# Kernel tuning notes

Hardware: AMD Instinct MI355X
Metric: run time of the kernel (lower is better)

Reference implementation:

```python
import jax, jax.numpy as jnp
import numpy as np


def _normalize_xyz_with_pc(pc, xyz):
    # Center by point-cloud centroid, scale by max radius of centered cloud.
    center = pc.mean(axis=1, keepdims=True)                      # [B,1,3]
    pc_c = pc - center
    scale = jnp.sqrt((pc_c ** 2).sum(-1)).max(axis=1)            # [B]
    scale = jnp.maximum(scale, 1e-6)[:, None, None]              # [B,1,1]
    return (xyz - center) / scale


def _nn_gather(seed_n, pts_n, feat):
    # seed_n [B,M,3], pts_n [B,K,3], feat [B,C,K] -> [B,C,M]
    d2 = ((seed_n ** 2).sum(-1)[:, :, None]
          + (pts_n ** 2).sum(-1)[:, None, :]
          - 2.0 * jnp.einsum('bmd,bkd->bmk', seed_n, pts_n))     # [B,M,K]
    idx = jnp.argmin(d2, axis=-1)                                # [B,M]
    return jnp.take_along_axis(feat, idx[:, None, :], axis=2)    # [B,C,M]


def _conv1x1(w, b, x):
    # w [O,C], b [O], x [B,C,M] -> [B,O,M]
    return jnp.einsum('oc,bcm->bom', w, x) + b[None, :, None]


def setup_inputs() -> dict:
    key = jax.random.key(0)
    ks = jax.random.split(key, 10)
    B, N, M, K, D = 4, 20000, 1024, 16384, 768
    return {
        'point_cloud': jax.random.normal(ks[0], (B, N, 3), jnp.float32),
        'seed_xyz': jax.random.normal(ks[1], (B, M, 3), jnp.float32),
        'seed_features': jax.random.normal(ks[2], (B, 256, M), jnp.float32),
        'pts': jax.random.normal(ks[3], (B, K, 3), jnp.float32),
        'feat': jax.random.normal(ks[4], (B, D, K), jnp.float32),
        'ln_gamma': jnp.ones((D,), jnp.float32),
        'ln_beta': jnp.zeros((D,), jnp.float32),
        'pw1': jax.random.normal(ks[5], (256, D), jnp.float32) * 0.02,
        'pb1': jnp.zeros((256,), jnp.float32),
        'pw2': jax.random.normal(ks[6], (256, 256), jnp.float32) * 0.02,
        'pb2': jnp.zeros((256,), jnp.float32),
        'fw1': jax.random.normal(ks[7], (256, 512), jnp.float32) * 0.02,
        'fb1': jnp.zeros((256,), jnp.float32),
        'fw2': jax.random.normal(ks[8], (256, 256), jnp.float32) * 0.02,
        'fb2': jnp.zeros((256,), jnp.float32),
    }


def reference(point_cloud, seed_xyz, seed_features, pts, feat,
              ln_gamma, ln_beta, pw1, pb1, pw2, pb2, fw1, fb1, fw2, fb2):
    seed_n = _normalize_xyz_with_pc(point_cloud, seed_xyz)       # [B,M,3]
    pts_n = _normalize_xyz_with_pc(point_cloud, pts)             # [B,K,3]
    vggt_raw = _nn_gather(seed_n, pts_n, feat)                   # [B,768,M]

    # LayerNorm over channel dim (applied on [B,M,768] in the original)
    x = vggt_raw.transpose(0, 2, 1)                              # [B,M,768]
    mu = x.mean(-1, keepdims=True)
    var = x.var(-1, keepdims=True)
    x_ln = ((x - mu) * jax.lax.rsqrt(var + 1e-5) * ln_gamma + ln_beta)
    x_ln = x_ln.transpose(0, 2, 1)                               # [B,768,M]

    vggt_proj = _conv1x1(pw2, pb2, jax.nn.relu(_conv1x1(pw1, pb1, x_ln)))
    fused = jnp.concatenate([seed_features, vggt_proj], axis=1)  # [B,512,M]
    mixed = _conv1x1(fw2, fb2, jax.nn.relu(_conv1x1(fw1, fb1, fused)))
    return mixed                                                 # [B,256,M]
```

## Files before the change

### kernel.cpp

```cpp
#include <hip/hip_runtime.h>
#include <math.h>

#define B_ 4
#define N_ 20000
#define M_ 1024
#define K_ 16384
#define D_ 768

typedef __attribute__((ext_vector_type(8))) short bf16x8;
typedef __attribute__((ext_vector_type(4))) float f32x4;

#define OFF_PART   0ul
#define OFF_RAD    1024ul
#define OFF_IDX    4096ul
#define OFF_P4     32768ul
#define OFF_NNP    1179648ul
#define OFF_G      2097152ul
#define OFF_XLN    16777216ul
#define OFF_FUSED  25165824ul
#define OFF_H2     29360128ul
#define OFF_WB1    33554432ul
#define OFF_WCAT   34603008ul
#define OFF_WB4    35651584ul
#define OFF_BC     36700160ul

__device__ inline unsigned short f2bf(float x) {
    union { float f; unsigned int u; } v; v.f = x;
    unsigned int r = v.u + 0x7fffu + ((v.u >> 16) & 1u);
    return (unsigned short)(r >> 16);
}

__device__ inline void gload_lds16(const void* g, void* lds) {
    __builtin_amdgcn_global_load_lds(
        (const __attribute__((address_space(1))) unsigned int*)g,
        (__attribute__((address_space(3))) unsigned int*)lds, 16, 0, 0);
}

__device__ inline void reduce_center(const float* part, int b,
                                     float& cx, float& cy, float& cz)
{
    cx = 0.f; cy = 0.f; cz = 0.f;
    #pragma unroll
    for (int r = 0; r < 16; ++r) {
        cx += part[(b*16+r)*3+0];
        cy += part[(b*16+r)*3+1];
        cz += part[(b*16+r)*3+2];
    }
    cx *= (1.f/N_); cy *= (1.f/N_); cz *= (1.f/N_);
}

__device__ inline float reduce_scale(const float* rad, int b)
{
    float m = 0.f;
    #pragma unroll
    for (int r = 0; r < 16; ++r) m = fmaxf(m, rad[b*16+r]);
    return fmaxf(sqrtf(m), 1e-6f);
}

__global__ __launch_bounds__(256) void k_pre(
    const float* __restrict__ pc,
    const float* __restrict__ pw1, const float* __restrict__ pw2,
    const float* __restrict__ pb2,
    const float* __restrict__ fw1, const float* __restrict__ fb1,
    const float* __restrict__ fw2,
    unsigned short* __restrict__ Wb1, unsigned short* __restrict__ Wcat,
    unsigned short* __restrict__ Wb4, float* __restrict__ bc,
    float* __restrict__ part)
{
    int bid = blockIdx.x, t = threadIdx.x;
    int lane = t & 63, wv = t >> 6;
    __shared__ float red[3][4];

    if (bid < 768) {
        int i0 = bid*256 + t;
        Wb1[i0] = f2bf(pw1[i0]);
        if (i0 < 65536) {
            int o = i0 >> 8, c = i0 & 255;
            Wcat[(size_t)o*512 + c] = f2bf(fw1[(size_t)o*512 + c]);
            Wb4[i0] = f2bf(fw2[i0]);
        }
    }
    if (bid < 256) {
        const float* fb = fw1 + (size_t)bid*512 + 256;
        float acc = 0.f;
        for (int j = 0; j < 256; ++j)
            acc = fmaf(fb[j], pw2[j*256 + t], acc);
        Wcat[(size_t)bid*512 + 256 + t] = f2bf(acc);
        float v = fb[t] * pb2[t];
        for (int off = 32; off; off >>= 1) v += __shfl_down(v, off, 64);
        if (!lane) red[0][wv] = v;
        __syncthreads();
        if (!t) bc[bid] = red[0][0]+red[0][1]+red[0][2]+red[0][3] + fb1[bid];
    } else if (bid >= 768) {
        int pi = bid - 768;
        int b = pi >> 4, chunk = pi & 15;
        const float* p = pc + (size_t)b * N_ * 3;
        int i0 = chunk * 1250;
        float sx = 0.f, sy = 0.f, sz = 0.f;
        for (int i = i0 + t; i < i0 + 1250; i += 256) {
            sx += p[i*3+0]; sy += p[i*3+1]; sz += p[i*3+2];
        }
        for (int off = 32; off; off >>= 1) {
            sx += __shfl_down(sx, off, 64);
            sy += __shfl_down(sy, off, 64);
            sz += __shfl_down(sz, off, 64);
        }
        if (!lane) { red[0][wv] = sx; red[1][wv] = sy; red[2][wv] = sz; }
        __syncthreads();
        if (!t) {
            part[(b*16+chunk)*3+0] = red[0][0]+red[0][1]+red[0][2]+red[0][3];
            part[(b*16+chunk)*3+1] = red[1][0]+red[1][1]+red[1][2]+red[1][3];
            part[(b*16+chunk)*3+2] = red[2][0]+red[2][1]+red[2][2]+red[2][3];
        }
    }
}

__global__ __launch_bounds__(256) void k_cs_rad(const float* __restrict__ pc,
                                                const float* __restrict__ part,
                                                float* __restrict__ rad)
{
    int blk = blockIdx.x, b = blk >> 4, pi = blk & 15;
    float cx, cy, cz;
    reduce_center(part, b, cx, cy, cz);
    const float* p = pc + (size_t)b * N_ * 3;
    int tid = threadIdx.x;
    int i0 = pi * 1250;
    float mx = 0.f;
    for (int i = i0 + tid; i < i0 + 1250; i += 256) {
        float dx = p[i*3+0]-cx, dy = p[i*3+1]-cy, dz = p[i*3+2]-cz;
        mx = fmaxf(mx, dx*dx + dy*dy + dz*dz);
    }
    for (int off = 32; off; off >>= 1) mx = fmaxf(mx, __shfl_down(mx, off, 64));
    __shared__ float red[4];
    int w = tid >> 6, l = tid & 63;
    if (!l) red[w] = mx;
    __syncthreads();
    if (!tid) rad[b*16+pi] = fmaxf(fmaxf(red[0], red[1]), fmaxf(red[2], red[3]));
}

__global__ __launch_bounds__(256) void k_prep_pts(const float* __restrict__ pts,
                                                  const float* __restrict__ part,
                                                  const float* __restrict__ rad,
                                                  float4* __restrict__ P4)
{
    int blk = blockIdx.x, b = blk >> 6;
    float cx, cy, cz;
    reduce_center(part, b, cx, cy, cz);
    float sc = 1.f / reduce_scale(rad, b);
    int k = (blk & 63)*256 + threadIdx.x;
    const float* pp = pts + ((size_t)b*K_ + k)*3;
    float px = (pp[0]-cx)*sc, py = (pp[1]-cy)*sc, pz = (pp[2]-cz)*sc;
    P4[(size_t)b*K_ + k] = make_float4(px, py, pz, px*px + py*py + pz*pz);
}

__global__ __launch_bounds__(256) void k_nn_part(const float* __restrict__ seed_xyz,
                                                 const float4* __restrict__ P4,
                                                 const float* __restrict__ part,
                                                 const float* __restrict__ rad,
                                                 float2* __restrict__ nnp)
{
    int blk = blockIdx.x;
    int ks = blk & 3, g = (blk >> 2) & 127, b = blk >> 9;
    float cx, cy, cz;
    reduce_center(part, b, cx, cy, cz);
    float scinv = 1.f / reduce_scale(rad, b);
    int t = threadIdx.x;
    int j = t & 31, s = t >> 5;
    int m = g*8 + s;
    const float* sp = seed_xyz + ((size_t)b*M_ + m)*3;
    float sx = (sp[0]-cx)*scinv, sy = (sp[1]-cy)*scinv, sz = (sp[2]-cz)*scinv;
    float ssq = sx*sx + sy*sy + sz*sz;
    const float4* Pb = P4 + (size_t)b*K_ + ks*4096;

    float best[4] = {3.4e38f, 3.4e38f, 3.4e38f, 3.4e38f};
    int   bk[4]   = {0, 0, 0, 0};
    for (int i = 0; i < 128; i += 4) {
        #pragma unroll
        for (int r = 0; r < 4; ++r) {
            int kk = (i + r)*32 + j;
            float4 q = Pb[kk];
            float d2 = ssq + q.w - 2.f*(sx*q.x + sy*q.y + sz*q.z);
            if (d2 < best[r]) { best[r] = d2; bk[r] = kk; }
        }
    }
    float bm = best[0]; int bmk = bk[0];
    #pragma unroll
    for (int r = 1; r < 4; ++r)
        if (best[r] < bm || (best[r] == bm && bk[r] < bmk)) { bm = best[r]; bmk = bk[r]; }
    #pragma unroll
    for (int mask = 16; mask; mask >>= 1) {
        float ob = __shfl_xor(bm, mask, 64);
        int   ok = __shfl_xor(bmk, mask, 64);
        if (ob < bm || (ob == bm && ok < bmk)) { bm = ob; bmk = ok; }
    }
    if (j == 0)
        nnp[((size_t)(b*M_ + m) << 2) + ks] = make_float2(bm, __int_as_float(ks*4096 + bmk));
}

__global__ __launch_bounds__(256) void k_nn_reduce(const float2* __restrict__ nnp,
                                                   int* __restrict__ idx)
{
    int i = blockIdx.x*256 + threadIdx.x;
    float bm = 3.4e38f; int bmk = 0;
    bool first = true;
    #pragma unroll
    for (int r = 0; r < 4; ++r) {
        float2 v = nnp[((size_t)i << 2) + r];
        int k = __float_as_int(v.y);
        if (first || v.x < bm || (v.x == bm && k < bmk)) { bm = v.x; bmk = k; first = false; }
    }
    idx[i] = bmk;
}

__global__ __launch_bounds__(256) void k_gather_tsf(const float* __restrict__ feat,
                                                    const int* __restrict__ idx,
                                                    const float* __restrict__ sf,
                                                    float* __restrict__ G,
                                                    unsigned short* __restrict__ fused)
{
    int bid = blockIdx.x, t = threadIdx.x;
    if (bid < 1536) {
        int b = bid / 384;
        int c = (bid - b*384) * 2;
        const float* frow0 = feat + ((size_t)b*D_ + c) * K_;
        const float* frow1 = frow0 + K_;
        const int* ib = idx + b*M_;
        float* g0 = G + ((size_t)b*D_ + c) * M_;
        float* g1 = g0 + M_;
        int id4[4];
        #pragma unroll
        for (int r = 0; r < 4; ++r) id4[r] = ib[r*256 + t];
        float v0[4], v1[4];
        #pragma unroll
        for (int r = 0; r < 4; ++r) v0[r] = frow0[id4[r]];
        #pragma unroll
        for (int r = 0; r < 4; ++r) v1[r] = frow1[id4[r]];
        #pragma unroll
        for (int r = 0; r < 4; ++r) g0[r*256 + t] = v0[r];
        #pragma unroll
        for (int r = 0; r < 4; ++r) g1[r*256 + t] = v1[r];
    } else {
        __shared__ float tile[32][33];
        int id = bid - 1536;
        int b = id >> 8, rem = id & 255;
        int m0 = (rem & 31) * 32, c0 = (rem >> 5) * 32;
        int tx = t & 31, ty = t >> 5;
        #pragma unroll
        for (int rr = 0; rr < 32; rr += 8)
            tile[ty+rr][tx] = sf[((size_t)b*256 + c0+ty+rr)*M_ + m0 + tx];
        __syncthreads();
        #pragma unroll
        for (int rr = 0; rr < 32; rr += 8)
            fused[((size_t)(b*M_ + m0+ty+rr))*512 + c0 + tx] = f2bf(tile[tx][ty+rr]);
    }
}

__global__ __launch_bounds__(256) void k_ln_fused(const float* __restrict__ G,
                                                  const float* __restrict__ gamma,
                                                  const float* __restrict__ beta,
                                                  unsigned short* __restrict__ xln)
{
    int b = blockIdx.y, m0 = blockIdx.x * 32;
    int t = threadIdx.x;
    int ml = t & 31, cp = t >> 5;
    const float* Gb = G + (size_t)b * D_ * M_;
    float s = 0.f, q = 0.f;
    for (int c = cp; c < D_; c += 8) {
        float v = Gb[(size_t)c*M_ + m0 + ml];
        s += v; q += v*v;
    }
    __shared__ float sred[8][32], qred[8][32];
    __shared__ float mu[32], iv[32];
    sred[cp][ml] = s; qred[cp][ml] = q;
    __syncthreads();
    if (t < 32) {
        float S = 0.f, Q = 0.f;
        #pragma unroll
        for (int r = 0; r < 8; ++r) { S += sred[r][t]; Q += qred[r][t]; }
        float m_ = S * (1.f/768.f);
        mu[t] = m_;
        iv[t] = rsqrtf(Q * (1.f/768.f) - m_*m_ + 1e-5f);
    }
    __syncthreads();

    __shared__ float tile[64][33];
    int ty = t >> 5;
    int cx2 = t & 31;
    for (int c0 = 0; c0 < D_; c0 += 64) {
        __syncthreads();
        #pragma unroll
        for (int ri = 0; ri < 8; ++ri) {
            int cl = ty*8 + ri;
            tile[cl][ml] = Gb[(size_t)(c0+cl)*M_ + m0 + ml];
        }
        __syncthreads();
        float2 ga = *(const float2*)&gamma[c0 + 2*cx2];
        float2 be = *(const float2*)&beta[c0 + 2*cx2];
        #pragma unroll
        for (int ri = 0; ri < 4; ++ri) {
            int m_l = ty*4 + ri;
            float v0 = (tile[2*cx2+0][m_l] - mu[m_l]) * iv[m_l] * ga.x + be.x;
            float v1 = (tile[2*cx2+1][m_l] - mu[m_l]) * iv[m_l] * ga.y + be.y;
            ushort2 pk = make_ushort2(f2bf(v0), f2bf(v1));
            *(ushort2*)&xln[((size_t)((b<<10) + m0 + m_l))*D_ + c0 + 2*cx2] = pk;
        }
    }
}

__global__ __launch_bounds__(256) void k_gemm_mfma(
    const unsigned short* __restrict__ X, const unsigned short* __restrict__ W,
    const float* __restrict__ bias, int Kdim, int relu, int mode,
    unsigned short* __restrict__ Ybf, int rowStride, int colOff,
    float* __restrict__ Yf)
{
    __shared__ unsigned short Al[2][64*64];
    __shared__ unsigned short Wl[2][64*64];
    int t = threadIdx.x, l = t & 63, w = t >> 6;
    int m0 = blockIdx.x * 64, o0 = blockIdx.y * 64;
    f32x4 acc[4];
    #pragma unroll
    for (int j = 0; j < 4; ++j) acc[j] = (f32x4){0.f, 0.f, 0.f, 0.f};

    int lin0 = w*1024;
    int lb0  = lin0 + l*16;
    int row0 = lb0 >> 7;
    int ks0  = ((lb0 >> 4) & 7) ^ (row0 & 7);
    int lin1 = 4096 + w*1024;
    int lb1  = lin1 + l*16;
    int row1 = lb1 >> 7;
    int ks1  = ((lb1 >> 4) & 7) ^ (row1 & 7);

    int nt = Kdim >> 6;

    gload_lds16(X + (size_t)(m0+row0)*Kdim + ks0*8, (char*)&Al[0][0] + lin0);
    gload_lds16(W + (size_t)(o0+row0)*Kdim + ks0*8, (char*)&Wl[0][0] + lin0);
    gload_lds16(X + (size_t)(m0+row1)*Kdim + ks1*8, (char*)&Al[0][0] + lin1);
    gload_lds16(W + (size_t)(o0+row1)*Kdim + ks1*8, (char*)&Wl[0][0] + lin1);
    __syncthreads();

    for (int tt = 0; tt < nt; ++tt) {
        int cur = tt & 1;
        if (tt + 1 < nt) {
            int kc = (tt + 1) << 6;
            gload_lds16(X + (size_t)(m0+row0)*Kdim + kc + ks0*8, (char*)&Al[cur^1][0] + lin0);
            gload_lds16(W + (size_t)(o0+row0)*Kdim + kc + ks0*8, (char*)&Wl[cur^1][0] + lin0);
            gload_lds16(X + (size_t)(m0+row1)*Kdim + kc + ks1*8, (char*)&Al[cur^1][0] + lin1);
            gload_lds16(W + (size_t)(o0+row1)*Kdim + kc + ks1*8, (char*)&Wl[cur^1][0] + lin1);
        }
        #pragma unroll
        for (int kk = 0; kk < 2; ++kk) {
            int arow = w*16 + (l & 15);
            int h = l >> 4;
            bf16x8 a = *(const bf16x8*)&Al[cur][arow*64 + (((kk<<2)|h) ^ (arow & 7))*8];
            #pragma unroll
            for (int j = 0; j < 4; ++j) {
                int orow = j*16 + (l & 15);
                bf16x8 bfr = *(const bf16x8*)&Wl[cur][orow*64 + (((kk<<2)|h) ^ (orow & 7))*8];
                acc[j] = __builtin_amdgcn_mfma_f32_16x16x32_bf16(a, bfr, acc[j], 0, 0, 0);
            }
        }
        __syncthreads();
    }

    int mbase = m0 + w*16 + (l >> 4)*4;
    if (mode == 0) {
        #pragma unroll
        for (int j = 0; j < 4; ++j) {
            int o = o0 + j*16 + (l & 15);
            float bi = bias[o];
            #pragma unroll
            for (int r = 0; r < 4; ++r) {
                float v = acc[j][r] + bi;
                if (relu) v = fmaxf(v, 0.f);
                Ybf[(size_t)(mbase + r)*rowStride + colOff + o] = f2bf(v);
            }
        }
    } else {
        int b = mbase >> 10, ml = mbase & 1023;
        #pragma unroll
        for (int j = 0; j < 4; ++j) {
            int o = o0 + j*16 + (l & 15);
            float bi = bias[o];
            float4 sv = make_float4(acc[j][0]+bi, acc[j][1]+bi, acc[j][2]+bi, acc[j][3]+bi);
            *(float4*)&Yf[((size_t)(b*256 + o))*1024 + ml] = sv;
        }
    }
}

extern "C" void kernel_launch(void* const* d_in, const int* in_sizes, int n_in,
                              void* d_out, int out_size, void* d_ws, size_t ws_size,
                              hipStream_t stream)
{
    (void)in_sizes; (void)n_in; (void)out_size; (void)ws_size;
    const float* pc        = (const float*)d_in[0];
    const float* seed_xyz  = (const float*)d_in[1];
    const float* seed_feat = (const float*)d_in[2];
    const float* pts       = (const float*)d_in[3];
    const float* feat      = (const float*)d_in[4];
    const float* ln_g      = (const float*)d_in[5];
    const float* ln_b      = (const float*)d_in[6];
    const float* pw1       = (const float*)d_in[7];
    const float* pb1       = (const float*)d_in[8];
    const float* pw2       = (const float*)d_in[9];
    const float* pb2       = (const float*)d_in[10];
    const float* fw1       = (const float*)d_in[11];
    const float* fb1       = (const float*)d_in[12];
    const float* fw2       = (const float*)d_in[13];
    const float* fb2       = (const float*)d_in[14];
    float* out = (float*)d_out;

    char* ws = (char*)d_ws;
    float*          part  = (float*)(ws + OFF_PART);
    float*          rad   = (float*)(ws + OFF_RAD);
    int*            idx   = (int*)(ws + OFF_IDX);
    float4*         P4    = (float4*)(ws + OFF_P4);
    float2*         nnp   = (float2*)(ws + OFF_NNP);
    float*          G     = (float*)(ws + OFF_G);
    unsigned short* xln   = (unsigned short*)(ws + OFF_XLN);
    unsigned short* fused = (unsigned short*)(ws + OFF_FUSED);
    unsigned short* h2    = (unsigned short*)(ws + OFF_H2);
    unsigned short* Wb1   = (unsigned short*)(ws + OFF_WB1);
    unsigned short* Wcat  = (unsigned short*)(ws + OFF_WCAT);
    unsigned short* Wb4   = (unsigned short*)(ws + OFF_WB4);
    float*          bc    = (float*)(ws + OFF_BC);

    k_pre<<<832, 256, 0, stream>>>(pc, pw1, pw2, pb2, fw1, fb1, fw2,
                                   Wb1, Wcat, Wb4, bc, part);
    k_cs_rad<<<64, 256, 0, stream>>>(pc, part, rad);
    k_prep_pts<<<256, 256, 0, stream>>>(pts, part, rad, P4);
    k_nn_part<<<2048, 256, 0, stream>>>(seed_xyz, P4, part, rad, nnp);
    k_nn_reduce<<<16, 256, 0, stream>>>(nnp, idx);
    k_gather_tsf<<<2560, 256, 0, stream>>>(feat, idx, seed_feat, G, fused);
    k_ln_fused<<<dim3(M_/32, B_), 256, 0, stream>>>(G, ln_g, ln_b, xln);
    k_gemm_mfma<<<dim3(64, 4), 256, 0, stream>>>(xln, Wb1, pb1, 768, 1, 0, fused, 512, 256, nullptr);
    k_gemm_mfma<<<dim3(64, 4), 256, 0, stream>>>(fused, Wcat, bc, 512, 1, 0, h2, 256, 0, nullptr);
    k_gemm_mfma<<<dim3(64, 4), 256, 0, stream>>>(h2, Wb4, fb2, 256, 0, 1, nullptr, 0, 0, out);
}
```

Measured before the change: 143.3 us.

## Sort NN indices per batch before gather and scatter LayerNorm rows by permutation

Result: slower. 186.6 us (+30.2%).

```diff
diff --git a/kernel.cpp b/kernel.cpp
--- a/kernel.cpp
+++ b/kernel.cpp
@@ -15,6 +15,8 @@
 #define OFF_IDX    4096ul
 #define OFF_P4     32768ul
 #define OFF_NNP    1179648ul
+#define OFF_SIDX   1310720ul
+#define OFF_SPERM  1331200ul
 #define OFF_G      2097152ul
 #define OFF_XLN    16777216ul
 #define OFF_FUSED  25165824ul
@@ -212,8 +214,39 @@
     idx[i] = bmk;
 }
 
+__global__ __launch_bounds__(256) void k_sort(const int* __restrict__ idx,
+                                              int* __restrict__ sidx,
+                                              int* __restrict__ sperm)
+{
+    __shared__ int key[1024];
+    __shared__ int val[1024];
+    int b = blockIdx.x, t = threadIdx.x;
+    for (int u = t; u < 1024; u += 256) { key[u] = idx[b*M_ + u]; val[u] = u; }
+    __syncthreads();
+    for (int k = 2; k <= 1024; k <<= 1) {
+        for (int jj = k >> 1; jj > 0; jj >>= 1) {
+            for (int u = t; u < 1024; u += 256) {
+                int p = u ^ jj;
+                if (p > u) {
+                    bool up = ((u & k) == 0);
+                    int ku = key[u], kp = key[p];
+                    if (up ? (ku > kp) : (ku < kp)) {
+                        key[u] = kp; key[p] = ku;
+                        int vu = val[u]; val[u] = val[p]; val[p] = vu;
+                    }
+                }
+            }
+            __syncthreads();
+        }
+    }
+    for (int u = t; u < 1024; u += 256) {
+        sidx[b*M_ + u]  = key[u];
+        sperm[b*M_ + u] = val[u];
+    }
+}
+
 __global__ __launch_bounds__(256) void k_gather_tsf(const float* __restrict__ feat,
-                                                    const int* __restrict__ idx,
+                                                    const int* __restrict__ sidx,
                                                     const float* __restrict__ sf,
                                                     float* __restrict__ G,
                                                     unsigned short* __restrict__ fused)
@@ -224,7 +257,7 @@
         int c = (bid - b*384) * 2;
         const float* frow0 = feat + ((size_t)b*D_ + c) * K_;
         const float* frow1 = frow0 + K_;
-        const int* ib = idx + b*M_;
+        const int* ib = sidx + b*M_;
         float* g0 = G + ((size_t)b*D_ + c) * M_;
         float* g1 = g0 + M_;
         int id4[4];
@@ -256,6 +289,7 @@
 }
 
 __global__ __launch_bounds__(256) void k_ln_fused(const float* __restrict__ G,
+                                                  const int* __restrict__ sperm,
                                                   const float* __restrict__ gamma,
                                                   const float* __restrict__ beta,
                                                   unsigned short* __restrict__ xln)
@@ -271,7 +305,9 @@
     }
     __shared__ float sred[8][32], qred[8][32];
     __shared__ float mu[32], iv[32];
+    __shared__ int prow[32];
     sred[cp][ml] = s; qred[cp][ml] = q;
+    if (t < 32) prow[t] = sperm[b*M_ + m0 + t];
     __syncthreads();
     if (t < 32) {
         float S = 0.f, Q = 0.f;
@@ -302,7 +338,7 @@
             float v0 = (tile[2*cx2+0][m_l] - mu[m_l]) * iv[m_l] * ga.x + be.x;
             float v1 = (tile[2*cx2+1][m_l] - mu[m_l]) * iv[m_l] * ga.y + be.y;
             ushort2 pk = make_ushort2(f2bf(v0), f2bf(v1));
-            *(ushort2*)&xln[((size_t)((b<<10) + m0 + m_l))*D_ + c0 + 2*cx2] = pk;
+            *(ushort2*)&xln[((size_t)((b<<10) + prow[m_l]))*D_ + c0 + 2*cx2] = pk;
         }
     }
 }
@@ -415,6 +451,8 @@
     int*            idx   = (int*)(ws + OFF_IDX);
     float4*         P4    = (float4*)(ws + OFF_P4);
     float2*         nnp   = (float2*)(ws + OFF_NNP);
+    int*            sidx  = (int*)(ws + OFF_SIDX);
+    int*            sperm = (int*)(ws + OFF_SPERM);
     float*          G     = (float*)(ws + OFF_G);
     unsigned short* xln   = (unsigned short*)(ws + OFF_XLN);
     unsigned short* fused = (unsigned short*)(ws + OFF_FUSED);
@@ -430,8 +468,9 @@
     k_prep_pts<<<256, 256, 0, stream>>>(pts, part, rad, P4);
     k_nn_part<<<2048, 256, 0, stream>>>(seed_xyz, P4, part, rad, nnp);
     k_nn_reduce<<<16, 256, 0, stream>>>(nnp, idx);
-    k_gather_tsf<<<2560, 256, 0, stream>>>(feat, idx, seed_feat, G, fused);
-    k_ln_fused<<<dim3(M_/32, B_), 256, 0, stream>>>(G, ln_g, ln_b, xln);
+    k_sort<<<4, 256, 0, stream>>>(idx, sidx, sperm);
+    k_gather_tsf<<<2560, 256, 0, stream>>>(feat, sidx, seed_feat, G, fused);
+    k_ln_fused<<<dim3(M_/32, B_), 256, 0, stream>>>(G, sperm, ln_g, ln_b, xln);
     k_gemm_mfma<<<dim3(64, 4), 256, 0, stream>>>(xln, Wb1, pb1, 768, 1, 0, fused, 512, 256, nullptr);
     k_gemm_mfma<<<dim3(64, 4), 256, 0, stream>>>(fused, Wcat, bc, 512, 1, 0, h2, 256, 0, nullptr);
     k_gemm_mfma<<<dim3(64, 4), 256, 0, stream>>>(h2, Wb4, fb2, 256, 0, 1, nullptr, 0, 0, out);
```

## Fold LayerNorm into first projection and run it before the gather

Applied to the files above, without the earlier changes.

Result: slower. 201.6 us (+40.7%).

```diff
diff --git a/kernel.cpp b/kernel.cpp
--- a/kernel.cpp
+++ b/kernel.cpp
@@ -15,14 +15,16 @@
 #define OFF_IDX    4096ul
 #define OFF_P4     32768ul
 #define OFF_NNP    1179648ul
-#define OFF_G      2097152ul
-#define OFF_XLN    16777216ul
-#define OFF_FUSED  25165824ul
-#define OFF_H2     29360128ul
-#define OFF_WB1    33554432ul
-#define OFF_WCAT   34603008ul
-#define OFF_WB4    35651584ul
-#define OFF_BC     36700160ul
+#define OFF_STATS  2097152ul
+#define OFF_AT     4194304ul
+#define OFF_FUSED  41943040ul
+#define OFF_H2     46137344ul
+#define OFF_WGB    50331648ul
+#define OFF_WCAT   51380224ul
+#define OFF_WB4    52428800ul
+#define OFF_BC     53477376ul
+#define OFF_S1     53481472ul
+#define OFF_BS2    53485568ul
 
 __device__ inline unsigned short f2bf(float x) {
     union { float f; unsigned int u; } v; v.f = x;
@@ -30,6 +32,11 @@
     return (unsigned short)(r >> 16);
 }
 
+__device__ inline float bf2f(unsigned short s) {
+    union { unsigned int u; float f; } v; v.u = ((unsigned int)s) << 16;
+    return v.f;
+}
+
 __device__ inline void gload_lds16(const void* g, void* lds) {
     __builtin_amdgcn_global_load_lds(
         (const __attribute__((address_space(1))) unsigned int*)g,
@@ -60,11 +67,13 @@
 __global__ __launch_bounds__(256) void k_pre(
     const float* __restrict__ pc,
     const float* __restrict__ pw1, const float* __restrict__ pw2,
-    const float* __restrict__ pb2,
+    const float* __restrict__ pb1, const float* __restrict__ pb2,
     const float* __restrict__ fw1, const float* __restrict__ fb1,
     const float* __restrict__ fw2,
-    unsigned short* __restrict__ Wb1, unsigned short* __restrict__ Wcat,
+    const float* __restrict__ ln_g, const float* __restrict__ ln_b,
+    unsigned short* __restrict__ wgb, unsigned short* __restrict__ Wcat,
     unsigned short* __restrict__ Wb4, float* __restrict__ bc,
+    float* __restrict__ s1, float* __restrict__ bs2,
     float* __restrict__ part)
 {
     int bid = blockIdx.x, t = threadIdx.x;
@@ -73,10 +82,11 @@
 
     if (bid < 768) {
         int i0 = bid*256 + t;
-        Wb1[i0] = f2bf(pw1[i0]);
+        int c = i0 % 768;
+        wgb[i0] = f2bf(pw1[i0] * ln_g[c]);
         if (i0 < 65536) {
-            int o = i0 >> 8, c = i0 & 255;
-            Wcat[(size_t)o*512 + c] = f2bf(fw1[(size_t)o*512 + c]);
+            int o = i0 >> 8, cc = i0 & 255;
+            Wcat[(size_t)o*512 + cc] = f2bf(fw1[(size_t)o*512 + cc]);
             Wb4[i0] = f2bf(fw2[i0]);
         }
     }
@@ -87,10 +97,27 @@
             acc = fmaf(fb[j], pw2[j*256 + t], acc);
         Wcat[(size_t)bid*512 + 256 + t] = f2bf(acc);
         float v = fb[t] * pb2[t];
-        for (int off = 32; off; off >>= 1) v += __shfl_down(v, off, 64);
-        if (!lane) red[0][wv] = v;
+        const float* po = pw1 + (size_t)bid*768;
+        float p1 = 0.f, p2 = 0.f;
+        #pragma unroll
+        for (int r = 0; r < 3; ++r) {
+            int c = r*256 + t;
+            float w = po[c];
+            p1 = fmaf(w, ln_g[c], p1);
+            p2 = fmaf(w, ln_b[c], p2);
+        }
+        for (int off = 32; off; off >>= 1) {
+            v  += __shfl_down(v, off, 64);
+            p1 += __shfl_down(p1, off, 64);
+            p2 += __shfl_down(p2, off, 64);
+        }
+        if (!lane) { red[0][wv] = v; red[1][wv] = p1; red[2][wv] = p2; }
         __syncthreads();
-        if (!t) bc[bid] = red[0][0]+red[0][1]+red[0][2]+red[0][3] + fb1[bid];
+        if (!t) {
+            bc[bid]  = red[0][0]+red[0][1]+red[0][2]+red[0][3] + fb1[bid];
+            s1[bid]  = red[1][0]+red[1][1]+red[1][2]+red[1][3];
+            bs2[bid] = red[2][0]+red[2][1]+red[2][2]+red[2][3] + pb1[bid];
+        }
     } else if (bid >= 768) {
         int pi = bid - 768;
         int b = pi >> 4, chunk = pi & 15;
@@ -111,6 +138,104 @@
             part[(b*16+chunk)*3+0] = red[0][0]+red[0][1]+red[0][2]+red[0][3];
             part[(b*16+chunk)*3+1] = red[1][0]+red[1][1]+red[1][2]+red[1][3];
             part[(b*16+chunk)*3+2] = red[2][0]+red[2][1]+red[2][2]+red[2][3];
+        }
+    }
+}
+
+__global__ __launch_bounds__(256) void k_gemmA(
+    const float* __restrict__ feat,
+    const unsigned short* __restrict__ wgb,
+    unsigned short* __restrict__ At,
+    float2* __restrict__ stats)
+{
+    __shared__ float Ft[64*64];
+    __shared__ unsigned short Wg[256*72];
+    __shared__ float sred[256], qred[256];
+    int blk = blockIdx.x;
+    int b = blk >> 8;
+    int k0 = (blk & 255) << 6;
+    int t = threadIdx.x, l = t & 63, w = t >> 6;
+
+    f32x4 acc[4][4];
+    #pragma unroll
+    for (int jo = 0; jo < 4; ++jo)
+        #pragma unroll
+        for (int jk = 0; jk < 4; ++jk)
+            acc[jo][jk] = (f32x4){0.f, 0.f, 0.f, 0.f};
+    float s_acc = 0.f, q_acc = 0.f;
+
+    const float* fb = feat + (size_t)b * D_ * K_ + k0;
+
+    for (int c0 = 0; c0 < D_; c0 += 64) {
+        __syncthreads();
+        #pragma unroll
+        for (int i = 0; i < 4; ++i) {
+            int c = i*16 + (t >> 4);
+            float4 v = *(const float4*)&fb[(size_t)(c0 + c) * K_ + (t & 15) * 4];
+            *(float4*)&Ft[c*64 + (t & 15)*4] = v;
+        }
+        #pragma unroll
+        for (int i = 0; i < 8; ++i) {
+            int o = i*32 + (t >> 3);
+            *(uint4*)&Wg[o*72 + (t & 7)*8] =
+                *(const uint4*)&wgb[(size_t)o*768 + c0 + (t & 7)*8];
+        }
+        __syncthreads();
+        {
+            int k = t & 63, pq = t >> 6;
+            #pragma unroll
+            for (int n = 0; n < 16; ++n) {
+                float v = Ft[(pq*16 + n)*64 + k];
+                s_acc += v; q_acc += v*v;
+            }
+        }
+        #pragma unroll
+        for (int kk = 0; kk < 2; ++kk) {
+            int g = (kk << 2) | (l >> 4);
+            bf16x8 bfr[4];
+            #pragma unroll
+            for (int jk = 0; jk < 4; ++jk) {
+                int k = jk*16 + (l & 15);
+                bf16x8 tmp;
+                #pragma unroll
+                for (int n = 0; n < 8; ++n)
+                    tmp[n] = (short)f2bf(Ft[(g*8 + n)*64 + k]);
+                bfr[jk] = tmp;
+            }
+            #pragma unroll
+            for (int jo = 0; jo < 4; ++jo) {
+                int orow = (w*4 + jo)*16 + (l & 15);
+                bf16x8 a = *(const bf16x8*)&Wg[orow*72 + g*8];
+                #pragma unroll
+                for (int jk = 0; jk < 4; ++jk)
+                    acc[jo][jk] = __builtin_amdgcn_mfma_f32_16x16x32_bf16(
+                        a, bfr[jk], acc[jo][jk], 0, 0, 0);
+            }
+        }
+    }
+    __syncthreads();
+    sred[t] = s_acc; qred[t] = q_acc;
+    __syncthreads();
+    if (t < 64) {
+        float S = sred[t] + sred[64+t] + sred[128+t] + sred[192+t];
+        float Q = qred[t] + qred[64+t] + qred[128+t] + qred[192+t];
+        float mu = S * (1.f/768.f);
+        float iv = rsqrtf(Q * (1.f/768.f) - mu*mu + 1e-5f);
+        stats[(size_t)b*K_ + k0 + t] = make_float2(mu, iv);
+    }
+    unsigned short* Ab = At + (size_t)b * K_ * 256;
+    #pragma unroll
+    for (int jo = 0; jo < 4; ++jo) {
+        int o = (w*4 + jo)*16 + ((l >> 4) << 2);
+        #pragma unroll
+        for (int jk = 0; jk < 4; ++jk) {
+            int k = jk*16 + (l & 15);
+            ushort4 pk;
+            pk.x = f2bf(acc[jo][jk][0]);
+            pk.y = f2bf(acc[jo][jk][1]);
+            pk.z = f2bf(acc[jo][jk][2]);
+            pk.w = f2bf(acc[jo][jk][3]);
+            *(ushort4*)&Ab[(size_t)(k0 + k)*256 + o] = pk;
         }
     }
 }
@@ -212,99 +337,55 @@
     idx[i] = bmk;
 }
 
-__global__ __launch_bounds__(256) void k_gather_tsf(const float* __restrict__ feat,
-                                                    const int* __restrict__ idx,
-                                                    const float* __restrict__ sf,
-                                                    float* __restrict__ G,
-                                                    unsigned short* __restrict__ fused)
+__global__ __launch_bounds__(256) void k_tsf(const float* __restrict__ sf,
+                                             unsigned short* __restrict__ fused)
+{
+    __shared__ float tile[32][33];
+    int id = blockIdx.x, t = threadIdx.x;
+    int b = id >> 8, rem = id & 255;
+    int m0 = (rem & 31) * 32, c0 = (rem >> 5) * 32;
+    int tx = t & 31, ty = t >> 5;
+    #pragma unroll
+    for (int rr = 0; rr < 32; rr += 8)
+        tile[ty+rr][tx] = sf[((size_t)b*256 + c0+ty+rr)*M_ + m0 + tx];
+    __syncthreads();
+    #pragma unroll
+    for (int rr = 0; rr < 32; rr += 8)
+        fused[((size_t)(b*M_ + m0+ty+rr))*512 + c0 + tx] = f2bf(tile[tx][ty+rr]);
+}
+
+__global__ __launch_bounds__(256) void k_combine(const int* __restrict__ idx,
+                                                 const unsigned short* __restrict__ At,
+                                                 const float2* __restrict__ stats,
+                                                 const float* __restrict__ s1,
+                                                 const float* __restrict__ bs2,
+                                                 unsigned short* __restrict__ fused)
 {
     int bid = blockIdx.x, t = threadIdx.x;
-    if (bid < 1536) {
-        int b = bid / 384;
-        int c = (bid - b*384) * 2;
-        const float* frow0 = feat + ((size_t)b*D_ + c) * K_;
-        const float* frow1 = frow0 + K_;
-        const int* ib = idx + b*M_;
-        float* g0 = G + ((size_t)b*D_ + c) * M_;
-        float* g1 = g0 + M_;
-        int id4[4];
-        #pragma unroll
-        for (int r = 0; r < 4; ++r) id4[r] = ib[r*256 + t];
-        float v0[4], v1[4];
-        #pragma unroll
-        for (int r = 0; r < 4; ++r) v0[r] = frow0[id4[r]];
-        #pragma unroll
-        for (int r = 0; r < 4; ++r) v1[r] = frow1[id4[r]];
-        #pragma unroll
-        for (int r = 0; r < 4; ++r) g0[r*256 + t] = v0[r];
-        #pragma unroll
-        for (int r = 0; r < 4; ++r) g1[r*256 + t] = v1[r];
-    } else {
-        __shared__ float tile[32][33];
-        int id = bid - 1536;
-        int b = id >> 8, rem = id & 255;
-        int m0 = (rem & 31) * 32, c0 = (rem >> 5) * 32;
-        int tx = t & 31, ty = t >> 5;
-        #pragma unroll
-        for (int rr = 0; rr < 32; rr += 8)
-            tile[ty+rr][tx] = sf[((size_t)b*256 + c0+ty+rr)*M_ + m0 + tx];
-        __syncthreads();
-        #pragma unroll
-        for (int rr = 0; rr < 32; rr += 8)
-            fused[((size_t)(b*M_ + m0+ty+rr))*512 + c0 + tx] = f2bf(tile[tx][ty+rr]);
-    }
-}
-
-__global__ __launch_bounds__(256) void k_ln_fused(const float* __restrict__ G,
-                                                  const float* __restrict__ gamma,
-                                                  const float* __restrict__ beta,
-                                                  unsigned short* __restrict__ xln)
-{
-    int b = blockIdx.y, m0 = blockIdx.x * 32;
-    int t = threadIdx.x;
-    int ml = t & 31, cp = t >> 5;
-    const float* Gb = G + (size_t)b * D_ * M_;
-    float s = 0.f, q = 0.f;
-    for (int c = cp; c < D_; c += 8) {
-        float v = Gb[(size_t)c*M_ + m0 + ml];
-        s += v; q += v*v;
-    }
-    __shared__ float sred[8][32], qred[8][32];
-    __shared__ float mu[32], iv[32];
-    sred[cp][ml] = s; qred[cp][ml] = q;
-    __syncthreads();
-    if (t < 32) {
-        float S = 0.f, Q = 0.f;
-        #pragma unroll
-        for (int r = 0; r < 8; ++r) { S += sred[r][t]; Q += qred[r][t]; }
-        float m_ = S * (1.f/768.f);
-        mu[t] = m_;
-        iv[t] = rsqrtf(Q * (1.f/768.f) - m_*m_ + 1e-5f);
-    }
-    __syncthreads();
-
-    __shared__ float tile[64][33];
-    int ty = t >> 5;
-    int cx2 = t & 31;
-    for (int c0 = 0; c0 < D_; c0 += 64) {
-        __syncthreads();
-        #pragma unroll
-        for (int ri = 0; ri < 8; ++ri) {
-            int cl = ty*8 + ri;
-            tile[cl][ml] = Gb[(size_t)(c0+cl)*M_ + m0 + ml];
-        }
-        __syncthreads();
-        float2 ga = *(const float2*)&gamma[c0 + 2*cx2];
-        float2 be = *(const float2*)&beta[c0 + 2*cx2];
-        #pragma unroll
-        for (int ri = 0; ri < 4; ++ri) {
-            int m_l = ty*4 + ri;
-            float v0 = (tile[2*cx2+0][m_l] - mu[m_l]) * iv[m_l] * ga.x + be.x;
-            float v1 = (tile[2*cx2+1][m_l] - mu[m_l]) * iv[m_l] * ga.y + be.y;
-            ushort2 pk = make_ushort2(f2bf(v0), f2bf(v1));
-            *(ushort2*)&xln[((size_t)((b<<10) + m0 + m_l))*D_ + c0 + 2*cx2] = pk;
-        }
-    }
+    int b = bid >> 7, grp = bid & 127;
+    int j = t & 31, s = t >> 5;
+    int m = grp*8 + s;
+    int k = idx[b*M_ + m];
+    float2 st = stats[(size_t)b*K_ + k];
+    const unsigned short* arow = At + ((size_t)b*K_ + k)*256 + j*8;
+    uint4 raw = *(const uint4*)arow;
+    const unsigned short* rs = (const unsigned short*)&raw;
+    float4 s1a = *(const float4*)&s1[j*8];
+    float4 s1b = *(const float4*)&s1[j*8 + 4];
+    float4 b2a = *(const float4*)&bs2[j*8];
+    float4 b2b = *(const float4*)&bs2[j*8 + 4];
+    float s1v[8] = {s1a.x, s1a.y, s1a.z, s1a.w, s1b.x, s1b.y, s1b.z, s1b.w};
+    float b2v[8] = {b2a.x, b2a.y, b2a.z, b2a.w, b2b.x, b2b.y, b2b.z, b2b.w};
+    ushort4 pk[2];
+    unsigned short* po = (unsigned short*)pk;
+    #pragma unroll
+    for (int e = 0; e < 8; ++e) {
+        float a = bf2f(rs[e]);
+        float h = fmaf(st.y, a - st.x * s1v[e], b2v[e]);
+        h = fmaxf(h, 0.f);
+        po[e] = f2bf(h);
+    }
+    *(uint4*)&fused[((size_t)(b*M_ + m))*512 + 256 + j*8] = *(uint4*)pk;
 }
 
 __global__ __launch_bounds__(256) void k_gemm_mfma(
@@ -415,24 +496,26 @@
     int*            idx   = (int*)(ws + OFF_IDX);
     float4*         P4    = (float4*)(ws + OFF_P4);
     float2*         nnp   = (float2*)(ws + OFF_NNP);
-    float*          G     = (float*)(ws + OFF_G);
-    unsigned short* xln   = (unsigned short*)(ws + OFF_XLN);
+    float2*         stats = (float2*)(ws + OFF_STATS);
+    unsigned short* At    = (unsigned short*)(ws + OFF_AT);
     unsigned short* fused = (unsigned short*)(ws + OFF_FUSED);
     unsigned short* h2    = (unsigned short*)(ws + OFF_H2);
-    unsigned short* Wb1   = (unsigned short*)(ws + OFF_WB1);
+    unsigned short* wgb   = (unsigned short*)(ws + OFF_WGB);
     unsigned short* Wcat  = (unsigned short*)(ws + OFF_WCAT);
     unsigned short* Wb4   = (unsigned short*)(ws + OFF_WB4);
     float*          bc    = (float*)(ws + OFF_BC);
-
-    k_pre<<<832, 256, 0, stream>>>(pc, pw1, pw2, pb2, fw1, fb1, fw2,
-                                   Wb1, Wcat, Wb4, bc, part);
+    float*          s1    = (float*)(ws + OFF_S1);
+    float*          bs2   = (float*)(ws + OFF_BS2);
+
+    k_pre<<<832, 256, 0, stream>>>(pc, pw1, pw2, pb1, pb2, fw1, fb1, fw2,
+                                   ln_g, ln_b, wgb, Wcat, Wb4, bc, s1, bs2, part);
+    k_gemmA<<<1024, 256, 0, stream>>>(feat, wgb, At, stats);
     k_cs_rad<<<64, 256, 0, stream>>>(pc, part, rad);
     k_prep_pts<<<256, 256, 0, stream>>>(pts, part, rad, P4);
     k_nn_part<<<2048, 256, 0, stream>>>(seed_xyz, P4, part, rad, nnp);
     k_nn_reduce<<<16, 256, 0, stream>>>(nnp, idx);
-    k_gather_tsf<<<2560, 256, 0, stream>>>(feat, idx, seed_feat, G, fused);
-    k_ln_fused<<<dim3(M_/32, B_), 256, 0, stream>>>(G, ln_g, ln_b, xln);
-    k_gemm_mfma<<<dim3(64, 4), 256, 0, stream>>>(xln, Wb1, pb1, 768, 1, 0, fused, 512, 256, nullptr);
+    k_tsf<<<1024, 256, 0, stream>>>(seed_feat, fused);
+    k_combine<<<512, 256, 0, stream>>>(idx, At, stats, s1, bs2, fused);
     k_gemm_mfma<<<dim3(64, 4), 256, 0, stream>>>(fused, Wcat, bc, 512, 1, 0, h2, 256, 0, nullptr);
     k_gemm_mfma<<<dim3(64, 4), 256, 0, stream>>>(h2, Wb4, fb2, 256, 0, 1, nullptr, 0, 0, out);
 }
```
